# Optimization experiments

Measured on AMD Instinct MI355X. Metric: run time of the kernel, lower is better.

The kernel has to match this reference:

```python
import jax, jax.numpy as jnp
import numpy as np

N, E, G, D, L = 150000, 150000, 128, 512, 5
MAX_DEPTH = 20
NUM_TYPES, NUM_ATTR = 98, 10030
EPS = 1e-5


def setup_inputs() -> dict:
    key = jax.random.key(0)
    k = jax.random.split(key, 24)

    def nrm(i, shape, s=0.05):
        return jax.random.normal(k[i], shape, dtype=jnp.float32) * s

    inp = {}
    inp["x"] = jax.random.randint(k[0], (N, 2), 0, NUM_TYPES)
    inp["node_depth"] = jax.random.randint(k[1], (N,), 0, 30)
    inp["edge_index"] = jax.random.randint(k[2], (2, E), 0, N)
    inp["batch"] = jnp.sort(jax.random.randint(k[3], (N,), 0, G)).at[0].set(0).at[-1].set(G - 1)
    inp["edge_attr"] = jax.random.normal(k[4], (E, 2), dtype=jnp.float32)
    inp["type_emb"] = nrm(5, (NUM_TYPES, D))
    inp["attr_emb"] = nrm(6, (NUM_ATTR, D))
    inp["depth_emb"] = nrm(7, (MAX_DEPTH + 1, D))
    inp["vn_w"] = jnp.zeros((1, D), jnp.float32)  # virtualnode_embedding initialized to zero
    inp["lin_w"] = nrm(8, (L, D, D))
    inp["lin_b"] = nrm(9, (L, D))
    inp["conv_bias"] = nrm(10, (L, D))
    inp["edge_w"] = nrm(11, (L, 2, D))
    inp["edge_b"] = nrm(12, (L, D))
    inp["bn_g"] = jnp.ones((L, D), jnp.float32)
    inp["bn_b"] = jnp.zeros((L, D), jnp.float32)
    inp["mlp_w1"] = nrm(13, (L - 1, D, 2 * D))
    inp["mlp_b1"] = nrm(14, (L - 1, 2 * D))
    inp["mlp_g"] = jnp.ones((L - 1, 2 * D), jnp.float32)
    inp["mlp_bb"] = jnp.zeros((L - 1, 2 * D), jnp.float32)
    inp["mlp_w2"] = nrm(15, (L - 1, 2 * D, D))
    inp["mlp_b2"] = nrm(16, (L - 1, D))
    return inp


def _bn(h, g, b):
    # training-mode BatchNorm1d: biased batch variance, eps=1e-5
    mu = h.mean(0)
    var = h.var(0)
    return (h - mu) * jax.lax.rsqrt(var + EPS) * g + b


def reference(x, node_depth, edge_index, batch, edge_attr, type_emb, attr_emb,
              depth_emb, vn_w, lin_w, lin_b, conv_bias, edge_w, edge_b,
              bn_g, bn_b, mlp_w1, mlp_b1, mlp_g, mlp_bb, mlp_w2, mlp_b2):
    # ASTNodeEncoder: sum of three embedding gathers, depth clamped to MAX_DEPTH
    depth = jnp.minimum(node_depth, MAX_DEPTH)
    h = type_emb[x[:, 0]] + attr_emb[x[:, 1]] + depth_emb[depth]  # [N, D]

    vn = jnp.broadcast_to(vn_w[0], (G, D))  # virtual node per graph

    row, col = edge_index[0], edge_index[1]  # messages flow row(source) -> col(target)
    deg = jax.ops.segment_sum(jnp.ones((E,), h.dtype), row, num_segments=N) + 1.0
    dis = deg ** -0.5
    norm = (dis[row] * dis[col])[:, None]  # [E, 1]

    for l in range(L):
        h = h + vn[batch]                      # virtual-node broadcast
        hx = h @ lin_w[l] + lin_b[l]           # [N, D]
        ee = edge_attr @ edge_w[l] + edge_b[l]  # [E, D]
        msg = norm * jax.nn.relu(hx[row] + ee)  # gather-compute
        agg = jax.ops.segment_sum(msg, col, num_segments=N)  # scatter-add
        h = agg + jax.nn.relu(hx + conv_bias[l]) / deg[:, None]
        h = _bn(h, bn_g[l], bn_b[l])
        if l == L - 1:
            break
        h = jax.nn.relu(h)
        vn = vn + jax.ops.segment_sum(h, batch, num_segments=G)  # global_add_pool
        z = jax.nn.relu(_bn(vn @ mlp_w1[l] + mlp_b1[l], mlp_g[l], mlp_bb[l]))
        vn = z @ mlp_w2[l] + mlp_b2[l]
    return h
```

## Files before the change

kernel.cpp:

```cpp
#include <hip/hip_runtime.h>
#include <hip/hip_bf16.h>
#include <stdint.h>

#define NN 150000
#define NE 150000
#define G 128
#define D 512
#define L 5
#define MAXD 20
#define EPS 1e-5f
#define NB ((NN + 255) / 256)

typedef unsigned short u16;
typedef unsigned int u32;
typedef __attribute__((ext_vector_type(8))) short bf16x8;
typedef __attribute__((ext_vector_type(4))) float f32x4;

__device__ __forceinline__ float bf2f(u16 u) {
    union { u32 i; float f; } v; v.i = ((u32)u) << 16; return v.f;
}
__device__ __forceinline__ u16 f2bf(float f) {
    union { float f; u32 i; } v; v.f = f;
    u32 r = v.i + 0x7FFF + ((v.i >> 16) & 1);
    return (u16)(r >> 16);
}
__device__ __forceinline__ void split2(float v, u16& hi, u16& lo) {
    hi = f2bf(v);
    lo = f2bf(v - bf2f(hi));
}

__device__ __forceinline__ void gload(const u16* g, u16* l) {
    __builtin_amdgcn_global_load_lds(
        (const __attribute__((address_space(1))) unsigned int*)g,
        (__attribute__((address_space(3))) unsigned int*)l, 16, 0, 0);
}

__global__ void k_zero(float* __restrict__ p, int n) {
    int i = blockIdx.x * 256 + threadIdx.x;
    if (i < n) p[i] = 0.0f;
}

__global__ void k_deg_count(const int* __restrict__ row, int* __restrict__ degint) {
    int e = blockIdx.x * 256 + threadIdx.x;
    if (e < NE) atomicAdd(&degint[row[e]], 1);
}
__global__ void k_deg_fin(const int* __restrict__ degint, float* __restrict__ deg,
                          float* __restrict__ dis) {
    int n = blockIdx.x * 256 + threadIdx.x;
    if (n < NN) {
        float d = (float)degint[n] + 1.0f;
        deg[n] = d;
        dis[n] = rsqrtf(d);
    }
}

__global__ void k_incount(const int* __restrict__ col, int* __restrict__ incnt) {
    int e = blockIdx.x * 256 + threadIdx.x;
    if (e < NE) atomicAdd(&incnt[col[e]], 1);
}
__global__ void k_scan1(const int* __restrict__ incnt, int* __restrict__ bsum) {
    __shared__ int sm[256];
    int b = blockIdx.x, t = threadIdx.x;
    int n = b * 256 + t;
    sm[t] = (n < NN) ? incnt[n] : 0;
    __syncthreads();
    #pragma unroll
    for (int s = 128; s > 0; s >>= 1) {
        if (t < s) sm[t] += sm[t + s];
        __syncthreads();
    }
    if (t == 0) bsum[b] = sm[0];
}
__global__ void k_scan2(const int* __restrict__ bsum, int* __restrict__ boff) {
    __shared__ int sm[1024];
    int t = threadIdx.x;
    int v0 = (t < NB) ? bsum[t] : 0;
    sm[t] = v0;
    __syncthreads();
    #pragma unroll
    for (int s = 1; s < 1024; s <<= 1) {
        int v = (t >= s) ? sm[t - s] : 0;
        __syncthreads();
        sm[t] += v;
        __syncthreads();
    }
    if (t < NB) boff[t] = sm[t] - v0;
}
__global__ void k_scan3(const int* __restrict__ incnt, const int* __restrict__ boff,
                        int* __restrict__ off, int* __restrict__ cursor) {
    __shared__ int sm[256];
    int b = blockIdx.x, t = threadIdx.x;
    int n = b * 256 + t;
    int c = (n < NN) ? incnt[n] : 0;
    sm[t] = c;
    __syncthreads();
    #pragma unroll
    for (int s = 1; s < 256; s <<= 1) {
        int v = (t >= s) ? sm[t - s] : 0;
        __syncthreads();
        sm[t] += v;
        __syncthreads();
    }
    if (n < NN) {
        int ex = boff[b] + sm[t] - c;
        off[n] = ex;
        cursor[n] = ex;
    }
}
__global__ void k_fill(const int* __restrict__ row, const int* __restrict__ col,
                       const float* __restrict__ ea, const float* __restrict__ dis,
                       int* __restrict__ cursor, float4* __restrict__ elist) {
    int e = blockIdx.x * 256 + threadIdx.x;
    if (e >= NE) return;
    int r = row[e], c = col[e];
    int pos = atomicAdd(&cursor[c], 1);
    float4 v;
    v.x = __int_as_float(r);
    v.y = dis[r] * dis[c];
    v.z = ea[2 * e];
    v.w = ea[2 * e + 1];
    elist[pos] = v;
}

__global__ void k_encoder(const int* __restrict__ x, const int* __restrict__ dep,
                          const float* __restrict__ te, const float* __restrict__ ae,
                          const float* __restrict__ de,
                          u16* __restrict__ hh, u16* __restrict__ hl) {
    int n = blockIdx.x, t = threadIdx.x;
    int t0 = x[2 * n], t1 = x[2 * n + 1];
    int dp = dep[n]; if (dp > MAXD) dp = MAXD;
    float2 a = ((const float2*)(te + (size_t)t0 * D))[t];
    float2 b = ((const float2*)(ae + (size_t)t1 * D))[t];
    float2 c = ((const float2*)(de + (size_t)dp * D))[t];
    float v0 = a.x + b.x + c.x;
    float v1 = a.y + b.y + c.y;
    u16 h0, l0, h1, l1;
    split2(v0, h0, l0); split2(v1, h1, l1);
    ((u32*)(hh + (size_t)n * D))[t] = (u32)h0 | ((u32)h1 << 16);
    ((u32*)(hl + (size_t)n * D))[t] = (u32)l0 | ((u32)l1 << 16);
}

__global__ void k_wsplit(const float* __restrict__ W, u16* __restrict__ Wh,
                         u16* __restrict__ Wl) {
    __shared__ float tile[32][33];
    int l = blockIdx.z, kt = blockIdx.y, nt = blockIdx.x;
    const float* Wlp = W + (size_t)l * D * D;
    int tx = threadIdx.x, ty = threadIdx.y;
    #pragma unroll
    for (int i = 0; i < 32; i += 8)
        tile[ty + i][tx] = Wlp[(size_t)(kt * 32 + ty + i) * D + nt * 32 + tx];
    __syncthreads();
    #pragma unroll
    for (int i = 0; i < 32; i += 8) {
        float v = tile[tx][ty + i];
        u16 hi, lo; split2(v, hi, lo);
        size_t o = (size_t)l * D * D + (size_t)(nt * 32 + ty + i) * D + kt * 32 + tx;
        Wh[o] = hi; Wl[o] = lo;
    }
}

__global__ void k_vninit(const float* __restrict__ vw, float* __restrict__ vn) {
    int i = blockIdx.x * 256 + threadIdx.x;
    vn[i] = vw[i & (D - 1)];
}

__global__ void k_vnw(const float* __restrict__ vn, const float* __restrict__ W,
                      const float* __restrict__ lb, float* __restrict__ vnW) {
    int g = blockIdx.x, c = threadIdx.x;
    __shared__ float sv[D];
    sv[c] = vn[g * D + c];
    __syncthreads();
    float acc = lb[c];
    for (int k = 0; k < D; k++) acc = fmaf(sv[k], W[(size_t)k * D + c], acc);
    vnW[g * D + c] = acc;
}

__global__ __launch_bounds__(256) void k_gemm3(
    const u16* __restrict__ Ahp, const u16* __restrict__ Alp,
    const u16* __restrict__ Bhp, const u16* __restrict__ Blp,
    const float* __restrict__ vnW, const int* __restrict__ batch,
    float* __restrict__ hx) {
    __shared__ __align__(16) u16 smem[4 * 4096];
    u16* sAh = smem;
    u16* sAl = smem + 4096;
    u16* sBh = smem + 8192;
    u16* sBl = smem + 12288;

    const int tid = threadIdx.x;
    const int wave = tid >> 6, ln = tid & 63;

    int wg = blockIdx.x;
    int gid = (wg & 7) * 586 + (wg >> 3);
    const long row0 = (long)(gid >> 2) * 128;
    const int col0 = (gid & 3) * 128;

    f32x4 acc[4][4] = {};
    const int wm = wave & 1, wn = wave >> 1;
    const int lrow = ln & 15, lq = ln >> 4;

    const int c1 = tid, c2 = tid + 256;
    long ar1 = row0 + (c1 & 127); if (ar1 >= NN) ar1 = NN - 1;
    long ar2 = row0 + (c2 & 127); if (ar2 >= NN) ar2 = NN - 1;
    const size_t aoff1 = (size_t)ar1 * D + (c1 >> 7) * 8;
    const size_t aoff2 = (size_t)ar2 * D + (c2 >> 7) * 8;
    const size_t boff1 = (size_t)(col0 + (c1 & 127)) * D + (c1 >> 7) * 8;
    const size_t boff2 = (size_t)(col0 + (c2 & 127)) * D + (c2 >> 7) * 8;
    u16* lA1 = sAh + c1 * 8;  u16* lA2 = sAh + c2 * 8;
    u16* lB1 = sAl + c1 * 8;  u16* lB2 = sAl + c2 * 8;
    u16* lC1 = sBh + c1 * 8;  u16* lC2 = sBh + c2 * 8;
    u16* lD1 = sBl + c1 * 8;  u16* lD2 = sBl + c2 * 8;

    for (int kt = 0; kt < D / 32; ++kt) {
        const int ks = kt * 32;
        __syncthreads();
        gload(Ahp + aoff1 + ks, lA1);
        gload(Ahp + aoff2 + ks, lA2);
        gload(Alp + aoff1 + ks, lB1);
        gload(Alp + aoff2 + ks, lB2);
        gload(Bhp + boff1 + ks, lC1);
        gload(Bhp + boff2 + ks, lC2);
        gload(Blp + boff1 + ks, lD1);
        gload(Blp + boff2 + ks, lD2);
        __syncthreads();

        bf16x8 ah[4], al[4], bh[4], bl[4];
        #pragma unroll
        for (int i = 0; i < 4; i++) {
            int ra = wm * 64 + i * 16 + lrow;
            int rb = wn * 64 + i * 16 + lrow;
            ah[i] = *(const bf16x8*)&sAh[lq * 1024 + ra * 8];
            al[i] = *(const bf16x8*)&sAl[lq * 1024 + ra * 8];
            bh[i] = *(const bf16x8*)&sBh[lq * 1024 + rb * 8];
            bl[i] = *(const bf16x8*)&sBl[lq * 1024 + rb * 8];
        }
        #pragma unroll
        for (int i = 0; i < 4; i++) {
            #pragma unroll
            for (int j = 0; j < 4; j++) {
                acc[i][j] = __builtin_amdgcn_mfma_f32_16x16x32_bf16(ah[i], bh[j], acc[i][j], 0, 0, 0);
                acc[i][j] = __builtin_amdgcn_mfma_f32_16x16x32_bf16(ah[i], bl[j], acc[i][j], 0, 0, 0);
                acc[i][j] = __builtin_amdgcn_mfma_f32_16x16x32_bf16(al[i], bh[j], acc[i][j], 0, 0, 0);
            }
        }
    }

    __syncthreads();
    float* fsm = (float*)smem;
    const int ep_off = wave * (32 * 64);
    const int rg = ln >> 4, cl = ln & 15;
    #pragma unroll
    for (int ip = 0; ip < 2; ip++) {
        #pragma unroll
        for (int i2 = 0; i2 < 2; i2++) {
            int i = ip * 2 + i2;
            #pragma unroll
            for (int j = 0; j < 4; j++) {
                #pragma unroll
                for (int r = 0; r < 4; r++) {
                    int srow = i2 * 16 + lq * 4 + r;
                    int m = (srow >> 2) & 3;
                    fsm[ep_off + srow * 64 + ((j ^ m) * 16) + lrow] = acc[i][j][r];
                }
            }
        }
        #pragma unroll
        for (int rr = 0; rr < 8; rr++) {
            int lr = rr * 4 + rg;
            int m = (lr >> 2) & 3;
            int sgrp = (cl >> 2) ^ m;
            long R = row0 + wm * 64 + ip * 32 + lr;
            if (R < NN) {
                float4 v = *(const float4*)&fsm[ep_off + lr * 64 + sgrp * 16 + (cl & 3) * 4];
                int Cc = col0 + wn * 64 + cl * 4;
                int g = batch[R];
                const float* vb = vnW + (size_t)g * D + Cc;
                float4 b4 = *(const float4*)vb;
                v.x += b4.x; v.y += b4.y; v.z += b4.z; v.w += b4.w;
                *(float4*)(hx + (size_t)R * D + Cc) = v;
            }
        }
        if (ip == 0) __syncthreads();
    }
}

__global__ __launch_bounds__(256) void k_aggr(
    const int* __restrict__ off, const int* __restrict__ cnt,
    const float4* __restrict__ elist, const float* __restrict__ hx,
    const float* __restrict__ cb, const float* __restrict__ deg,
    const float* __restrict__ ew, const float* __restrict__ eb,
    float* __restrict__ out, float* __restrict__ bns) {
    const int lane = threadIdx.x & 63;
    const int wv = threadIdx.x >> 6;
    const int gw = blockIdx.x * 4 + wv;
    const int nwaves = gridDim.x * 4;
    const int c0 = lane * 8;

    float w0[8], w1[8], bb[8], cbv[8];
    *(float4*)&w0[0] = *(const float4*)(ew + c0);
    *(float4*)&w0[4] = *(const float4*)(ew + c0 + 4);
    *(float4*)&w1[0] = *(const float4*)(ew + D + c0);
    *(float4*)&w1[4] = *(const float4*)(ew + D + c0 + 4);
    *(float4*)&bb[0] = *(const float4*)(eb + c0);
    *(float4*)&bb[4] = *(const float4*)(eb + c0 + 4);
    *(float4*)&cbv[0] = *(const float4*)(cb + c0);
    *(float4*)&cbv[4] = *(const float4*)(cb + c0 + 4);

    float s[8] = {}, q[8] = {};

    for (int n = gw; n < NN; n += nwaves) {
        float a[8];
        const float* hp = hx + (size_t)n * D + c0;
        *(float4*)&a[0] = *(const float4*)(hp);
        *(float4*)&a[4] = *(const float4*)(hp + 4);
        float invd = 1.0f / deg[n];
        float acc8[8];
        #pragma unroll
        for (int j = 0; j < 8; j++) acc8[j] = fmaxf(a[j] + cbv[j], 0.0f) * invd;

        int k0 = off[n], k1 = k0 + cnt[n];
        for (int k = k0; k < k1; k++) {
            float4 m = elist[k];
            int r = __float_as_int(m.x);
            const float* hr = hx + (size_t)r * D + c0;
            float hf[8];
            *(float4*)&hf[0] = *(const float4*)(hr);
            *(float4*)&hf[4] = *(const float4*)(hr + 4);
            #pragma unroll
            for (int j = 0; j < 8; j++)
                acc8[j] = fmaf(m.y, fmaxf(hf[j] + fmaf(m.z, w0[j], fmaf(m.w, w1[j], bb[j])), 0.0f), acc8[j]);
        }
        float* op = out + (size_t)n * D + c0;
        *(float4*)(op) = *(const float4*)&acc8[0];
        *(float4*)(op + 4) = *(const float4*)&acc8[4];
        #pragma unroll
        for (int j = 0; j < 8; j++) {
            s[j] += acc8[j];
            q[j] = fmaf(acc8[j], acc8[j], q[j]);
        }
    }

    __shared__ float red[4][512];
    #pragma unroll
    for (int j = 0; j < 8; j++) red[wv][c0 + j] = s[j];
    __syncthreads();
    if (wv == 0) {
        #pragma unroll
        for (int j = 0; j < 8; j++) {
            int c = c0 + j;
            float t = red[0][c] + red[1][c] + red[2][c] + red[3][c];
            atomicAdd(&bns[c], t);
        }
    }
    __syncthreads();
    #pragma unroll
    for (int j = 0; j < 8; j++) red[wv][c0 + j] = q[j];
    __syncthreads();
    if (wv == 0) {
        #pragma unroll
        for (int j = 0; j < 8; j++) {
            int c = c0 + j;
            float t = red[0][c] + red[1][c] + red[2][c] + red[3][c];
            atomicAdd(&bns[D + c], t);
        }
    }
}

__global__ void k_bnfin(const float* __restrict__ sums, const float* __restrict__ g,
                        const float* __restrict__ b, float* __restrict__ sc,
                        float* __restrict__ sh) {
    int c = threadIdx.x;
    float mu = sums[c] * (1.0f / NN);
    float var = fmaxf(sums[D + c] * (1.0f / NN) - mu * mu, 0.0f);
    float rstd = rsqrtf(var + EPS);
    float scale = rstd * g[c];
    sc[c] = scale;
    sh[c] = b[c] - mu * scale;
}

__global__ void k_final(const float* __restrict__ accb, const float* __restrict__ sc,
                        const float* __restrict__ sh, const int* __restrict__ batch,
                        u16* __restrict__ hh, u16* __restrict__ hl,
                        float* __restrict__ pool) {
    int t = threadIdx.x; int c = 2 * t;
    long n0 = (long)blockIdx.x * 256;
    float s0 = sc[c], s1 = sc[c + 1], h0 = sh[c], h1 = sh[c + 1];
    float p0 = 0, p1 = 0; int gc = -1;
    for (int rI = 0; rI < 256; rI++) {
        long n = n0 + rI; if (n >= NN) break;
        float2 v = *(const float2*)(accb + (size_t)n * D + c);
        float a = fmaxf(fmaf(v.x, s0, h0), 0.0f);
        float b = fmaxf(fmaf(v.y, s1, h1), 0.0f);
        u16 ah, al, bh, bl;
        split2(a, ah, al); split2(b, bh, bl);
        ((u32*)(hh + (size_t)n * D))[t] = (u32)ah | ((u32)bh << 16);
        ((u32*)(hl + (size_t)n * D))[t] = (u32)al | ((u32)bl << 16);
        int g = batch[n];
        if (g != gc) {
            if (gc >= 0) { atomicAdd(&pool[gc * D + c], p0); atomicAdd(&pool[gc * D + c + 1], p1); }
            gc = g; p0 = 0; p1 = 0;
        }
        p0 += a; p1 += b;
    }
    if (gc >= 0) { atomicAdd(&pool[gc * D + c], p0); atomicAdd(&pool[gc * D + c + 1], p1); }
}

__global__ void k_finalout(const float* __restrict__ accb, const float* __restrict__ sc,
                           const float* __restrict__ sh, float* __restrict__ out) {
    int t = threadIdx.x; int c = 2 * t;
    long n0 = (long)blockIdx.x * 256;
    float s0 = sc[c], s1 = sc[c + 1], h0 = sh[c], h1 = sh[c + 1];
    for (int rI = 0; rI < 256; rI++) {
        long n = n0 + rI; if (n >= NN) break;
        float2 v = *(const float2*)(accb + (size_t)n * D + c);
        ((float2*)out)[n * 256 + t] = make_float2(fmaf(v.x, s0, h0), fmaf(v.y, s1, h1));
    }
}

__global__ void k_mlp1(const float* __restrict__ vn, const float* __restrict__ pool,
                       const float* __restrict__ w1, const float* __restrict__ b1,
                       float* __restrict__ u) {
    int g = blockIdx.x >> 2;
    int j = ((blockIdx.x & 3) << 8) | threadIdx.x;
    __shared__ float sv[D];
    int t = threadIdx.x;
    sv[t] = vn[g * D + t] + pool[g * D + t];
    sv[t + 256] = vn[g * D + t + 256] + pool[g * D + t + 256];
    __syncthreads();
    float acc = b1[j];
    for (int k = 0; k < D; k++) acc = fmaf(sv[k], w1[(size_t)k * 2 * D + j], acc);
    u[(size_t)g * 2 * D + j] = acc;
}
__global__ void k_mbn(const float* __restrict__ u, const float* __restrict__ mg,
                      const float* __restrict__ mb, float* __restrict__ z) {
    int j = blockIdx.x * 256 + threadIdx.x;
    float s = 0, q = 0;
    for (int g = 0; g < G; g++) { float v = u[(size_t)g * 2 * D + j]; s += v; q = fmaf(v, v, q); }
    float mu = s * (1.0f / G);
    float var = fmaxf(q * (1.0f / G) - mu * mu, 0.0f);
    float rstd = rsqrtf(var + EPS);
    float sc = rstd * mg[j];
    float sh = mb[j] - mu * sc;
    for (int g = 0; g < G; g++)
        z[(size_t)g * 2 * D + j] = fmaxf(fmaf(u[(size_t)g * 2 * D + j], sc, sh), 0.0f);
}
__global__ void k_mlp2(const float* __restrict__ z, const float* __restrict__ w2,
                       const float* __restrict__ b2, float* __restrict__ vn) {
    int g = blockIdx.x >> 1;
    int c = ((blockIdx.x & 1) << 8) | threadIdx.x;
    __shared__ float sz[2 * D];
    int t = threadIdx.x;
    #pragma unroll
    for (int i = 0; i < 4; i++) sz[t + i * 256] = z[(size_t)g * 2 * D + t + i * 256];
    __syncthreads();
    float acc = b2[c];
    for (int k = 0; k < 2 * D; k++) acc = fmaf(sz[k], w2[(size_t)k * D + c], acc);
    vn[g * D + c] = acc;
}

extern "C" void kernel_launch(void* const* d_in, const int* in_sizes, int n_in,
                              void* d_out, int out_size, void* d_ws, size_t ws_size,
                              hipStream_t stream) {
    (void)in_sizes; (void)n_in; (void)out_size; (void)ws_size;
    const int*   x     = (const int*)d_in[0];
    const int*   ndep  = (const int*)d_in[1];
    const int*   ei    = (const int*)d_in[2];
    const int*   batch = (const int*)d_in[3];
    const float* ea    = (const float*)d_in[4];
    const float* te    = (const float*)d_in[5];
    const float* ae    = (const float*)d_in[6];
    const float* de    = (const float*)d_in[7];
    const float* vw    = (const float*)d_in[8];
    const float* lw    = (const float*)d_in[9];
    const float* lb    = (const float*)d_in[10];
    const float* cb    = (const float*)d_in[11];
    const float* ew    = (const float*)d_in[12];
    const float* ebp   = (const float*)d_in[13];
    const float* bng   = (const float*)d_in[14];
    const float* bnb   = (const float*)d_in[15];
    const float* mw1   = (const float*)d_in[16];
    const float* mb1   = (const float*)d_in[17];
    const float* mg    = (const float*)d_in[18];
    const float* mbb   = (const float*)d_in[19];
    const float* mw2   = (const float*)d_in[20];
    const float* mb2   = (const float*)d_in[21];

    char* ws = (char*)d_ws;
    size_t off_ = 0;
    auto alloc = [&](size_t b) { size_t o = off_; off_ += (b + 255) & ~(size_t)255; return o; };
    u16*  hh   = (u16*)(ws + alloc((size_t)NN * D * 2));
    u16*  hl   = (u16*)(ws + alloc((size_t)NN * D * 2));
    float* hx  = (float*)(ws + alloc((size_t)NN * D * 4));
    float* acc = (float*)(ws + alloc((size_t)NN * D * 4));
    u16*  Wth  = (u16*)(ws + alloc((size_t)L * D * D * 2));
    u16*  Wtl  = (u16*)(ws + alloc((size_t)L * D * D * 2));
    float* vnW = (float*)(ws + alloc((size_t)G * D * 4));
    float* vn  = (float*)(ws + alloc((size_t)G * D * 4));
    float* pool= (float*)(ws + alloc((size_t)G * D * 4));
    float* u   = (float*)(ws + alloc((size_t)G * 2 * D * 4));
    float* z   = (float*)(ws + alloc((size_t)G * 2 * D * 4));
    float* deg = (float*)(ws + alloc((size_t)NN * 4));
    float* dis = (float*)(ws + alloc((size_t)NN * 4));
    int* degint= (int*)(ws + alloc((size_t)NN * 4));
    float* bns = (float*)(ws + alloc((size_t)2 * D * 4));
    float* bsc = (float*)(ws + alloc((size_t)D * 4));
    float* bsh = (float*)(ws + alloc((size_t)D * 4));
    int* incnt  = (int*)(ws + alloc((size_t)NN * 4));
    int* offp   = (int*)(ws + alloc((size_t)NN * 4));
    int* cursor = (int*)(ws + alloc((size_t)NN * 4));
    int* bsum   = (int*)(ws + alloc((size_t)1024 * 4));
    int* boff   = (int*)(ws + alloc((size_t)1024 * 4));
    float4* elist = (float4*)(ws + alloc((size_t)NE * 16));

    const int* row = ei;
    const int* colp = ei + NE;

    k_zero<<<(NN + 255) / 256, 256, 0, stream>>>((float*)degint, NN);
    k_deg_count<<<(NE + 255) / 256, 256, 0, stream>>>(row, degint);
    k_deg_fin<<<(NN + 255) / 256, 256, 0, stream>>>(degint, deg, dis);

    k_zero<<<(NN + 255) / 256, 256, 0, stream>>>((float*)incnt, NN);
    k_incount<<<(NE + 255) / 256, 256, 0, stream>>>(colp, incnt);
    k_scan1<<<NB, 256, 0, stream>>>(incnt, bsum);
    k_scan2<<<1, 1024, 0, stream>>>(bsum, boff);
    k_scan3<<<NB, 256, 0, stream>>>(incnt, boff, offp, cursor);
    k_fill<<<(NE + 255) / 256, 256, 0, stream>>>(row, colp, ea, dis, cursor, elist);

    k_encoder<<<NN, 256, 0, stream>>>(x, ndep, te, ae, de, hh, hl);
    k_wsplit<<<dim3(16, 16, L), dim3(32, 8), 0, stream>>>(lw, Wth, Wtl);
    k_vninit<<<G * D / 256, 256, 0, stream>>>(vw, vn);

    for (int l = 0; l < L; l++) {
        k_vnw<<<G, 512, 0, stream>>>(vn, lw + (size_t)l * D * D, lb + (size_t)l * D, vnW);
        k_gemm3<<<dim3(4688), 256, 0, stream>>>(
            hh, hl, Wth + (size_t)l * D * D, Wtl + (size_t)l * D * D, vnW, batch, hx);
        k_zero<<<4, 256, 0, stream>>>(bns, 2 * D);
        k_aggr<<<2048, 256, 0, stream>>>(offp, incnt, elist, hx, cb + (size_t)l * D,
                                         deg, ew + (size_t)l * 2 * D,
                                         ebp + (size_t)l * D, acc, bns);
        k_bnfin<<<1, D, 0, stream>>>(bns, bng + (size_t)l * D, bnb + (size_t)l * D, bsc, bsh);
        if (l < L - 1) {
            k_zero<<<G * D / 256, 256, 0, stream>>>(pool, G * D);
            k_final<<<(NN + 255) / 256, 256, 0, stream>>>(acc, bsc, bsh, batch, hh, hl, pool);
            k_mlp1<<<G * 4, 256, 0, stream>>>(vn, pool, mw1 + (size_t)l * D * 2 * D,
                                              mb1 + (size_t)l * 2 * D, u);
            k_mbn<<<4, 256, 0, stream>>>(u, mg + (size_t)l * 2 * D, mbb + (size_t)l * 2 * D, z);
            k_mlp2<<<G * 2, 256, 0, stream>>>(z, mw2 + (size_t)l * 2 * D * D,
                                              mb2 + (size_t)l * D, vn);
        } else {
            k_finalout<<<(NN + 255) / 256, 256, 0, stream>>>(acc, bsc, bsh, (float*)d_out);
        }
    }
}
```

Before: 6.269 ms.

## Store GEMM output as bf16 hi/lo pair and gather only hi in aggregation

The GEMM epilogue now writes hx as two bf16 arrays (high and low parts) instead of fp32. The self term in aggregation rebuilds full precision from hi+lo, while neighbor gathers read only the bf16 high part, halving gather bytes. It also prefetches the next edge record and uses nontemporal stores and loads for streaming data. Gathered neighbor features lose precision, down to bf16, which may affect accuracy.

```diff
diff --git a/kernel.cpp b/kernel.cpp
--- a/kernel.cpp
+++ b/kernel.cpp
@@ -15,6 +15,8 @@
 typedef unsigned int u32;
 typedef __attribute__((ext_vector_type(8))) short bf16x8;
 typedef __attribute__((ext_vector_type(4))) float f32x4;
+typedef __attribute__((ext_vector_type(4))) u32 u32x4;
+typedef __attribute__((ext_vector_type(2))) u32 u32x2;
 
 __device__ __forceinline__ float bf2f(u16 u) {
     union { u32 i; float f; } v; v.i = ((u32)u) << 16; return v.f;
@@ -179,7 +181,7 @@
     const u16* __restrict__ Ahp, const u16* __restrict__ Alp,
     const u16* __restrict__ Bhp, const u16* __restrict__ Blp,
     const float* __restrict__ vnW, const int* __restrict__ batch,
-    float* __restrict__ hx) {
+    u16* __restrict__ hxh, u16* __restrict__ hxl) {
     __shared__ __align__(16) u16 smem[4 * 4096];
     u16* sAh = smem;
     u16* sAl = smem + 4096;
@@ -276,7 +278,13 @@
                 const float* vb = vnW + (size_t)g * D + Cc;
                 float4 b4 = *(const float4*)vb;
                 v.x += b4.x; v.y += b4.y; v.z += b4.z; v.w += b4.w;
-                *(float4*)(hx + (size_t)R * D + Cc) = v;
+                u16 h0, l0, h1, l1, h2, l2, h3, l3;
+                split2(v.x, h0, l0); split2(v.y, h1, l1);
+                split2(v.z, h2, l2); split2(v.w, h3, l3);
+                u32x2 ph2 = { (u32)h0 | ((u32)h1 << 16), (u32)h2 | ((u32)h3 << 16) };
+                u32x2 pl2 = { (u32)l0 | ((u32)l1 << 16), (u32)l2 | ((u32)l3 << 16) };
+                *(u32x2*)(hxh + (size_t)R * D + Cc) = ph2;
+                __builtin_nontemporal_store(pl2, (u32x2*)(hxl + (size_t)R * D + Cc));
             }
         }
         if (ip == 0) __syncthreads();
@@ -285,7 +293,8 @@
 
 __global__ __launch_bounds__(256) void k_aggr(
     const int* __restrict__ off, const int* __restrict__ cnt,
-    const float4* __restrict__ elist, const float* __restrict__ hx,
+    const float4* __restrict__ elist, const u16* __restrict__ hxh,
+    const u16* __restrict__ hxl,
     const float* __restrict__ cb, const float* __restrict__ deg,
     const float* __restrict__ ew, const float* __restrict__ eb,
     float* __restrict__ out, float* __restrict__ bns) {
@@ -308,30 +317,37 @@
     float s[8] = {}, q[8] = {};
 
     for (int n = gw; n < NN; n += nwaves) {
-        float a[8];
-        const float* hp = hx + (size_t)n * D + c0;
-        *(float4*)&a[0] = *(const float4*)(hp);
-        *(float4*)&a[4] = *(const float4*)(hp + 4);
+        u32x4 ph = *(const u32x4*)(hxh + (size_t)n * D + c0);
+        u32x4 pl = __builtin_nontemporal_load((const u32x4*)(hxl + (size_t)n * D + c0));
         float invd = 1.0f / deg[n];
         float acc8[8];
         #pragma unroll
-        for (int j = 0; j < 8; j++) acc8[j] = fmaxf(a[j] + cbv[j], 0.0f) * invd;
-
-        int k0 = off[n], k1 = k0 + cnt[n];
-        for (int k = k0; k < k1; k++) {
-            float4 m = elist[k];
-            int r = __float_as_int(m.x);
-            const float* hr = hx + (size_t)r * D + c0;
-            float hf[8];
-            *(float4*)&hf[0] = *(const float4*)(hr);
-            *(float4*)&hf[4] = *(const float4*)(hr + 4);
-            #pragma unroll
-            for (int j = 0; j < 8; j++)
-                acc8[j] = fmaf(m.y, fmaxf(hf[j] + fmaf(m.z, w0[j], fmaf(m.w, w1[j], bb[j])), 0.0f), acc8[j]);
+        for (int j = 0; j < 8; j++) {
+            float hi = bf2f((u16)(ph[j >> 1] >> ((j & 1) * 16)));
+            float lo = bf2f((u16)(pl[j >> 1] >> ((j & 1) * 16)));
+            acc8[j] = fmaxf(hi + lo + cbv[j], 0.0f) * invd;
+        }
+
+        int k0 = off[n], kc = cnt[n];
+        if (kc > 0) {
+            float4 m = elist[k0];
+            for (int k = 0; k < kc; k++) {
+                float4 mn = (k + 1 < kc) ? elist[k0 + k + 1] : m;
+                int r = __float_as_int(m.x);
+                u32x4 g4 = *(const u32x4*)(hxh + (size_t)r * D + c0);
+                #pragma unroll
+                for (int j = 0; j < 8; j++) {
+                    float hf = bf2f((u16)(g4[j >> 1] >> ((j & 1) * 16)));
+                    acc8[j] = fmaf(m.y, fmaxf(hf + fmaf(m.z, w0[j], fmaf(m.w, w1[j], bb[j])), 0.0f), acc8[j]);
+                }
+                m = mn;
+            }
         }
         float* op = out + (size_t)n * D + c0;
-        *(float4*)(op) = *(const float4*)&acc8[0];
-        *(float4*)(op + 4) = *(const float4*)&acc8[4];
+        f32x4 o0 = { acc8[0], acc8[1], acc8[2], acc8[3] };
+        f32x4 o1 = { acc8[4], acc8[5], acc8[6], acc8[7] };
+        __builtin_nontemporal_store(o0, (f32x4*)op);
+        __builtin_nontemporal_store(o1, (f32x4*)(op + 4));
         #pragma unroll
         for (int j = 0; j < 8; j++) {
             s[j] += acc8[j];
@@ -489,7 +505,8 @@
     auto alloc = [&](size_t b) { size_t o = off_; off_ += (b + 255) & ~(size_t)255; return o; };
     u16*  hh   = (u16*)(ws + alloc((size_t)NN * D * 2));
     u16*  hl   = (u16*)(ws + alloc((size_t)NN * D * 2));
-    float* hx  = (float*)(ws + alloc((size_t)NN * D * 4));
+    u16*  hxh  = (u16*)(ws + alloc((size_t)NN * D * 2));
+    u16*  hxl  = (u16*)(ws + alloc((size_t)NN * D * 2));
     float* acc = (float*)(ws + alloc((size_t)NN * D * 4));
     u16*  Wth  = (u16*)(ws + alloc((size_t)L * D * D * 2));
     u16*  Wtl  = (u16*)(ws + alloc((size_t)L * D * D * 2));
@@ -532,9 +549,9 @@
     for (int l = 0; l < L; l++) {
         k_vnw<<<G, 512, 0, stream>>>(vn, lw + (size_t)l * D * D, lb + (size_t)l * D, vnW);
         k_gemm3<<<dim3(4688), 256, 0, stream>>>(
-            hh, hl, Wth + (size_t)l * D * D, Wtl + (size_t)l * D * D, vnW, batch, hx);
+            hh, hl, Wth + (size_t)l * D * D, Wtl + (size_t)l * D * D, vnW, batch, hxh, hxl);
         k_zero<<<4, 256, 0, stream>>>(bns, 2 * D);
-        k_aggr<<<2048, 256, 0, stream>>>(offp, incnt, elist, hx, cb + (size_t)l * D,
+        k_aggr<<<2048, 256, 0, stream>>>(offp, incnt, elist, hxh, hxl, cb + (size_t)l * D,
                                          deg, ew + (size_t)l * 2 * D,
                                          ebp + (size_t)l * D, acc, bns);
         k_bnfin<<<1, D, 0, stream>>>(bns, bng + (size_t)l * D, bnb + (size_t)l * D, bsc, bsh);
```

After: 6.296 ms. About the same (+0.4%).
